# Performance work log

Hardware: AMD Instinct MI355X
Metric: run time of the kernel (lower is better)

## Reference

```python
import jax, jax.numpy as jnp
import numpy as np
from jax import lax


def _conv2d(x, w, pad=1):
    # x: (N,C,H,W), w: (O,I,kh,kw) -> (N,O,H,W)
    return lax.conv_general_dilated(
        x, w, window_strides=(1, 1), padding=[(pad, pad), (pad, pad)],
        dimension_numbers=("NCHW", "OIHW", "NCHW"))


def setup_inputs() -> dict:
    key = jax.random.key(0)
    ks = jax.random.split(key, 5)
    B, T, C, H, W = 4, 8, 256, 64, 64
    DH = 128
    fan = C * 3 * 3
    x = jax.random.normal(ks[0], (B, T, C, H, W), dtype=jnp.float32)
    w_k = jax.random.normal(ks[1], (DH, C, 3, 3), dtype=jnp.float32) * (2.0 / fan) ** 0.5
    w_q = jax.random.normal(ks[2], (DH, C, 3, 3), dtype=jnp.float32) * (2.0 / fan) ** 0.5
    w_v = jax.random.normal(ks[3], (DH, C, 3, 3), dtype=jnp.float32) * (2.0 / fan) ** 0.5
    w_out = jax.random.normal(ks[4], (C, DH, 3, 3), dtype=jnp.float32) * (2.0 / (DH * 9)) ** 0.5
    b_out = jnp.zeros((C,), dtype=jnp.float32)
    return {"x": x, "w_k": w_k, "w_q": w_q, "w_v": w_v, "w_out": w_out, "b_out": b_out}


def reference(x, w_k, w_q, w_v, w_out, b_out):
    B, T, C, H, W = x.shape
    DH = w_k.shape[0]
    # key comes only from the first frame
    k = _conv2d(x[:, 0], w_k)                                  # (B,DH,H,W)
    xf = x.reshape(B * T, C, H, W)
    q = _conv2d(xf, w_q).reshape(B, T, DH, H, W)               # (B,T,DH,H,W)
    v = _conv2d(xf, w_v).reshape(B, T, DH, H, W)
    # per-pixel channel dot between each frame's q and the single k
    dots = jnp.einsum("btchw,bchw->bthw", q, k)                # (B,T,H,W)
    attn = jax.nn.softmax(dots, axis=1)                        # softmax over T
    pooled = jnp.einsum("bthw,btchw->bchw", attn, v)           # (B,DH,H,W)
    # out conv applied once (result is identical for every repeated frame)
    out = _conv2d(pooled, w_out) + b_out[None, :, None, None]  # (B,C,H,W)
    return jnp.broadcast_to(out[:, None], (B, T, C, H, W))
```

## Files before the change

kernel.cpp:

```cpp
#include <hip/hip_runtime.h>
#include <cstdint>
#include <cstddef>

#define NB 4
#define NT 8
#define NC 256
#define NDH 128
#define HWs 4096

typedef _Float16 f16;
typedef _Float16 f16x8 __attribute__((ext_vector_type(8)));
typedef float f32x16 __attribute__((ext_vector_type(16)));


__device__ __forceinline__ void gload16(const void* g, void* l) {
    __builtin_amdgcn_global_load_lds(
        (const __attribute__((address_space(1))) void*)g,
        (__attribute__((address_space(3))) void*)l, 16, 0, 0);
}

__device__ __forceinline__ int xcd_swz(int bid, int nwg) {
    int q = nwg >> 3;
    return (bid & 7) * q + (bid >> 3);
}

__global__ __launch_bounds__(256) void prep_x_kernel(const float* __restrict__ x,
                                                     f16* __restrict__ xh) {
    __shared__ f16 sxt[256 * 66];
    int bt = blockIdx.x >> 6, h = blockIdx.x & 63;
    int tid = threadIdx.x;
    int w = tid & 63, c4 = tid >> 6;
    for (int p = 0; p < 64; ++p) {
        int c = p * 4 + c4;
        sxt[c * 66 + w] = (f16)x[(((size_t)bt * NC + c) * 64 + h) * 64 + w];
    }
    __syncthreads();
    int cg = tid & 31, wb = tid >> 5;
    f16x8* xh8 = (f16x8*)xh;
    for (int p = 0; p < 8; ++p) {
        int w2 = wb * 8 + p;
        f16x8 v;
        #pragma unroll
        for (int j = 0; j < 8; ++j) v[j] = sxt[(cg * 8 + j) * 66 + w2];
        xh8[((size_t)(bt * 64 + h) * 64 + w2) * 32 + cg] = v;
    }
}

__global__ __launch_bounds__(256) void prep_w_kernel(const float* __restrict__ w,
                                                     f16* __restrict__ wt2,
                                                     int OC, int CIN) {
    int CG = CIN >> 3;
    int idx = blockIdx.x * 256 + threadIdx.x;
    if (idx >= OC * CG) return;
    int oc = idx / CG, cg = idx - oc * CG;
    f16x8* wt8 = (f16x8*)wt2;
    #pragma unroll
    for (int tap = 0; tap < 9; ++tap) {
        f16x8 v;
        #pragma unroll
        for (int j = 0; j < 8; ++j)
            v[j] = (f16)w[((size_t)oc * CIN + cg * 8 + j) * 9 + tap];
        wt8[((size_t)tap * CG + cg) * OC + oc] = v;
    }
}

template <int CIN>
__device__ __forceinline__ void conv_core4(const f16x8* __restrict__ xh8,
                                           const f16x8* __restrict__ wt8,
                                           int OCT, int oc0, int h0,
                                           f16x8* __restrict__ sxb,
                                           f16x8* __restrict__ swb,
                                           f32x16 acc[2][2][2]) {
    const int tid = threadIdx.x;
    const int lane = tid & 63;
    const int wv = tid >> 6;
    const int ocg = wv >> 2, rp = wv & 3;
    const int n = lane & 31, q = lane >> 5;
    const int CG = CIN / 8;
    const int NI = CIN / 16;

    #pragma unroll
    for (int oi = 0; oi < 2; ++oi)
        #pragma unroll
        for (int rr = 0; rr < 2; ++rr)
            #pragma unroll
            for (int ct = 0; ct < 2; ++ct)
                #pragma unroll
                for (int r = 0; r < 16; ++r) acc[oi][rr][ct][r] = 0.0f;

    f16x8 Z8 = {(f16)0, (f16)0, (f16)0, (f16)0, (f16)0, (f16)0, (f16)0, (f16)0};

    if (tid < 80) {
        int buf = tid / 40, rem = tid - buf * 40;
        int r = rem >> 2, k = rem & 3;
        sxb[buf * 1320 + r * 132 + (k >> 1) * 130 + (k & 1)] = Z8;
    }
    if (h0 == 0 && tid < 264) {
        int buf = tid / 132, c = tid - buf * 132;
        sxb[buf * 1320 + c] = Z8;
    }
    if (h0 == 56 && tid < 264) {
        int buf = tid / 132, c = tid - buf * 132;
        sxb[buf * 1320 + 9 * 132 + c] = Z8;
    }

    auto stage = [&](f16x8* sx8, f16x8* sw8, int cg0) {
        for (int j = wv; j < 36; j += 8) {
            int tap = j >> 2, qh = (j >> 1) & 1, hf = j & 1;
            gload16(wt8 + (size_t)(tap * CG + cg0 + qh) * OCT + oc0 + hf * 64 + lane,
                    sw8 + (tap * 2 + qh) * 128 + hf * 64);
        }
        for (int j = wv; j < 20; j += 8) {
            int r = j >> 1, cb = j & 1;
            int h = h0 - 1 + r;
            if ((unsigned)h < 64u) {
                int col = cb * 32 + (lane >> 1);
                int cidx = col + 1;
                int cg = cg0 + ((lane & 1) ^ ((cidx >> 2) & 1));
                gload16(xh8 + (size_t)(h * 64 + col) * CG + cg,
                        sx8 + r * 132 + 2 + cb * 64);
            }
        }
    };

    stage(sxb, swb, 0);
    __syncthreads();

    for (int it = 0; it < NI; ++it) {
        f16x8* sx8 = sxb + (it & 1) * 1320;
        f16x8* sw8 = swb + (it & 1) * 2304;
        if (it + 1 < NI)
            stage(sxb + ((it + 1) & 1) * 1320, swb + ((it + 1) & 1) * 2304,
                  (it + 1) * 2);

        __builtin_amdgcn_s_setprio(1);
        #pragma unroll
        for (int kx = 0; kx < 3; ++kx) {
            f16x8 bb[4][2];
            #pragma unroll
            for (int j = 0; j < 4; ++j) {
                const int r = rp * 2 + j;
                #pragma unroll
                for (int ct = 0; ct < 2; ++ct) {
                    int cidx = ct * 32 + n + kx;
                    int s = q ^ ((cidx >> 2) & 1);
                    bb[j][ct] = sx8[r * 132 + cidx * 2 + s];
                }
            }
            #pragma unroll
            for (int ky = 0; ky < 3; ++ky) {
                const int tap = ky * 3 + kx;
                f16x8 a0 = sw8[(tap * 2 + q) * 128 + ocg * 64 + n];
                f16x8 a1 = sw8[(tap * 2 + q) * 128 + ocg * 64 + 32 + n];
                #pragma unroll
                for (int rr = 0; rr < 2; ++rr) {
                    #pragma unroll
                    for (int ct = 0; ct < 2; ++ct) {
                        f16x8 b = bb[rr + ky][ct];
                        acc[0][rr][ct] = __builtin_amdgcn_mfma_f32_32x32x16_f16(a0, b, acc[0][rr][ct], 0, 0, 0);
                        acc[1][rr][ct] = __builtin_amdgcn_mfma_f32_32x32x16_f16(a1, b, acc[1][rr][ct], 0, 0, 0);
                    }
                }
            }
        }
        __builtin_amdgcn_s_setprio(0);
        __syncthreads();
    }
}

__global__ __launch_bounds__(512, 2) void conv_k_kernel(const f16* __restrict__ xh,
        const f16* __restrict__ wk2, float* __restrict__ kbuf) {
    __shared__ f16x8 sxb[2 * 1320];
    __shared__ f16x8 swb[2 * 2304];
    int s = xcd_swz(blockIdx.x, NB * 8);
    int b = s >> 3, hb = s & 7;
    int h0 = hb * 8;
    int bt = b * NT;
    f32x16 acc[2][2][2];
    conv_core4<NC>((const f16x8*)xh + (size_t)bt * 64 * 64 * 32, (const f16x8*)wk2,
                   NDH, 0, h0, sxb, swb, acc);
    int lane = threadIdx.x & 63, wv = threadIdx.x >> 6;
    int ocg = wv >> 2, rp = wv & 3;
    int n = lane & 31, q = lane >> 5;
    #pragma unroll
    for (int rr = 0; rr < 2; ++rr) {
        int h = h0 + rp * 2 + rr;
        #pragma unroll
        for (int oi = 0; oi < 2; ++oi)
            #pragma unroll
            for (int r = 0; r < 16; ++r) {
                int oc = ocg * 64 + oi * 32 + 4 * q + (r & 3) + 8 * (r >> 2);
                float* kp = kbuf + ((size_t)(b * NDH + oc)) * HWs + h * 64;
                kp[n] = acc[oi][rr][0][r];
                kp[32 + n] = acc[oi][rr][1][r];
            }
    }
}

__global__ __launch_bounds__(512, 2) void conv_q_kernel(const f16* __restrict__ xh,
        const f16* __restrict__ wq2, const float* __restrict__ kbuf,
        float* __restrict__ qpart) {
    __shared__ f16x8 sxb[2 * 1320];
    __shared__ f16x8 swb[2 * 2304];
    int s = xcd_swz(blockIdx.x, NB * NT * 8);
    int bt = s >> 3, hb = s & 7;
    int b = bt >> 3;
    int h0 = hb * 8;
    f32x16 acc[2][2][2];
    conv_core4<NC>((const f16x8*)xh + (size_t)bt * 64 * 64 * 32, (const f16x8*)wq2,
                   NDH, 0, h0, sxb, swb, acc);
    int lane = threadIdx.x & 63, wv = threadIdx.x >> 6;
    int ocg = wv >> 2, rp = wv & 3;
    int n = lane & 31, q = lane >> 5;
    #pragma unroll
    for (int rr = 0; rr < 2; ++rr) {
        int h = h0 + rp * 2 + rr;
        float p0 = 0.0f, p1 = 0.0f;
        #pragma unroll
        for (int oi = 0; oi < 2; ++oi)
            #pragma unroll
            for (int r = 0; r < 16; ++r) {
                int oc = ocg * 64 + oi * 32 + 4 * q + (r & 3) + 8 * (r >> 2);
                const float* kp = kbuf + ((size_t)(b * NDH + oc)) * HWs + h * 64;
                p0 += acc[oi][rr][0][r] * kp[n];
                p1 += acc[oi][rr][1][r] * kp[32 + n];
            }
        p0 += __shfl_xor(p0, 32, 64);
        p1 += __shfl_xor(p1, 32, 64);
        if (q == 0) {
            qpart[((size_t)ocg * 32 + bt) * HWs + h * 64 + n] = p0;
            qpart[((size_t)ocg * 32 + bt) * HWs + h * 64 + 32 + n] = p1;
        }
    }
}

__global__ __launch_bounds__(256) void softmax_t_kernel(const float* __restrict__ qpart,
                                                        float* __restrict__ dots) {
    int idx = blockIdx.x * 256 + threadIdx.x;
    int b = idx >> 12;
    int p = idx & 4095;
    const float* q0 = qpart + (size_t)(b * NT) * HWs + p;
    const float* q1 = qpart + (size_t)(32 + b * NT) * HWs + p;
    float v[NT];
    float m = -3.4e38f;
    #pragma unroll
    for (int t = 0; t < NT; ++t) { v[t] = q0[t * HWs] + q1[t * HWs]; m = fmaxf(m, v[t]); }
    float s = 0.0f;
    #pragma unroll
    for (int t = 0; t < NT; ++t) { v[t] = __expf(v[t] - m); s += v[t]; }
    float inv = 1.0f / s;
    float* base = dots + (size_t)b * NT * HWs + p;
    #pragma unroll
    for (int t = 0; t < NT; ++t) base[t * HWs] = v[t] * inv;
}

__global__ __launch_bounds__(512, 2) void conv_v_kernel(const f16* __restrict__ xh,
        const f16* __restrict__ wv2, const float* __restrict__ attn,
        f16* __restrict__ parts) {
    __shared__ f16x8 sxb[2 * 1320];
    __shared__ f16x8 swb[2 * 2304];
    int s = xcd_swz(blockIdx.x, NB * NT * 8);
    int bt = s >> 3, hb = s & 7;
    int b = bt >> 3, t = bt & 7;
    int h0 = hb * 8;
    f32x16 acc[2][2][2];
    conv_core4<NC>((const f16x8*)xh + (size_t)bt * 64 * 64 * 32, (const f16x8*)wv2,
                   NDH, 0, h0, sxb, swb, acc);
    int lane = threadIdx.x & 63, wv = threadIdx.x >> 6;
    int ocg = wv >> 2, rp = wv & 3;
    int n = lane & 31, q = lane >> 5;
    f16* pp = parts + (size_t)(t * NB + b) * NDH * HWs;
    #pragma unroll
    for (int rr = 0; rr < 2; ++rr) {
        int h = h0 + rp * 2 + rr;
        float a0 = attn[(size_t)bt * HWs + h * 64 + n];
        float a1 = attn[(size_t)bt * HWs + h * 64 + 32 + n];
        #pragma unroll
        for (int oi = 0; oi < 2; ++oi)
            #pragma unroll
            for (int r = 0; r < 16; ++r) {
                int oc = ocg * 64 + oi * 32 + 4 * q + (r & 3) + 8 * (r >> 2);
                f16* op = pp + (size_t)oc * HWs + h * 64;
                op[n] = (f16)(a0 * acc[oi][rr][0][r]);
                op[32 + n] = (f16)(a1 * acc[oi][rr][1][r]);
            }
    }
}

__global__ __launch_bounds__(256) void prep_pooled_kernel(const f16* __restrict__ parts,
                                                          f16* __restrict__ pooledT) {
    __shared__ f16 sxt[128 * 66];
    int b = blockIdx.x >> 6, h = blockIdx.x & 63;
    int tid = threadIdx.x, w = tid & 63, c4 = tid >> 6;
    for (int p = 0; p < 32; ++p) {
        int c = p * 4 + c4;
        float s = 0.0f;
        #pragma unroll
        for (int t = 0; t < NT; ++t)
            s += (float)parts[(((size_t)(t * NB + b) * NDH + c)) * HWs + h * 64 + w];
        sxt[c * 66 + w] = (f16)s;
    }
    __syncthreads();
    int cg = tid & 15, wb = tid >> 4;
    f16x8* pt8 = (f16x8*)pooledT;
    for (int p = 0; p < 4; ++p) {
        int w2 = wb * 4 + p;
        f16x8 v;
        #pragma unroll
        for (int j = 0; j < 8; ++j) v[j] = sxt[(cg * 8 + j) * 66 + w2];
        pt8[((size_t)(b * 64 + h) * 64 + w2) * 16 + cg] = v;
    }
}

__global__ __launch_bounds__(512, 2) void conv_out_kernel(const f16* __restrict__ pooledT,
        const f16* __restrict__ wo2, const float* __restrict__ b_out,
        float* __restrict__ out) {
    __shared__ f16x8 sxb[2 * 1320];
    __shared__ f16x8 swb[2 * 2304];
    int s = xcd_swz(blockIdx.x, NB * 2 * 8);
    int b = s >> 4, oh = (s >> 3) & 1, hb = s & 7;
    int h0 = hb * 8, oc0 = oh * 128;
    f32x16 acc[2][2][2];
    conv_core4<NDH>((const f16x8*)pooledT + (size_t)b * 64 * 64 * 16, (const f16x8*)wo2,
                    NC, oc0, h0, sxb, swb, acc);
    int lane = threadIdx.x & 63, wv = threadIdx.x >> 6;
    int ocg = wv >> 2, rp = wv & 3;
    int n = lane & 31, q = lane >> 5;
    #pragma unroll
    for (int rr = 0; rr < 2; ++rr) {
        int h = h0 + rp * 2 + rr;
        #pragma unroll
        for (int oi = 0; oi < 2; ++oi)
            #pragma unroll
            for (int r = 0; r < 16; ++r) {
                int oc = oc0 + ocg * 64 + oi * 32 + 4 * q + (r & 3) + 8 * (r >> 2);
                float bias = b_out[oc];
                float v0 = acc[oi][rr][0][r] + bias;
                float v1 = acc[oi][rr][1][r] + bias;
                for (int t = 0; t < NT; ++t) {
                    float* op = out + ((size_t)(b * NT + t) * NC + oc) * HWs + h * 64;
                    op[n] = v0;
                    op[32 + n] = v1;
                }
            }
    }
}

extern "C" void kernel_launch(void* const* d_in, const int* in_sizes, int n_in,
                              void* d_out, int out_size, void* d_ws, size_t ws_size,
                              hipStream_t stream) {
    (void)in_sizes; (void)n_in; (void)out_size; (void)ws_size;
    const float* x     = (const float*)d_in[0];
    const float* w_k   = (const float*)d_in[1];
    const float* w_q   = (const float*)d_in[2];
    const float* w_v   = (const float*)d_in[3];
    const float* w_out = (const float*)d_in[4];
    const float* b_out = (const float*)d_in[5];
    float* out = (float*)d_out;

    char* ws = (char*)d_ws;
    f16*   xh      = (f16*)ws;
    float* kbuf    = (float*)(ws + 67108864);
    float* dots    = (float*)(ws + 75497472);
    f16*   parts   = (f16*)(ws + 76021760);
    float* qpart   = (float*)(ws + 76021760);
    f16*   pooledT = (f16*)(ws + 109576192);
    f16*   wq2     = (f16*)(ws + 113770496);
    f16*   wk2     = (f16*)(ws + 114360320);
    f16*   wv2     = (f16*)(ws + 114950144);
    f16*   wo2     = (f16*)(ws + 115539968);

    hipLaunchKernelGGL(prep_x_kernel, dim3(2048), dim3(256), 0, stream, x, xh);
    hipLaunchKernelGGL(prep_w_kernel, dim3(16), dim3(256), 0, stream, w_q, wq2, NDH, NC);
    hipLaunchKernelGGL(prep_w_kernel, dim3(16), dim3(256), 0, stream, w_k, wk2, NDH, NC);
    hipLaunchKernelGGL(prep_w_kernel, dim3(16), dim3(256), 0, stream, w_v, wv2, NDH, NC);
    hipLaunchKernelGGL(prep_w_kernel, dim3(16), dim3(256), 0, stream, w_out, wo2, NC, NDH);

    hipLaunchKernelGGL(conv_k_kernel, dim3(NB * 8), dim3(512), 0, stream, xh, wk2, kbuf);
    hipLaunchKernelGGL(conv_q_kernel, dim3(NB * NT * 8), dim3(512), 0, stream, xh, wq2, kbuf, qpart);
    hipLaunchKernelGGL(softmax_t_kernel, dim3(64), dim3(256), 0, stream, qpart, dots);
    hipLaunchKernelGGL(conv_v_kernel, dim3(NB * NT * 8), dim3(512), 0, stream, xh, wv2, dots, parts);
    hipLaunchKernelGGL(prep_pooled_kernel, dim3(256), dim3(256), 0, stream, parts, pooledT);
    hipLaunchKernelGGL(conv_out_kernel, dim3(NB * 2 * 8), dim3(512), 0, stream, pooledT, wo2, b_out, out);
}
```

Before: 540.6 us.

## Split-K the key conv across blocks and double-buffer B fragments in conv core

The key conv previously ran on only 32 blocks. It is now split four ways over input channels into 128 blocks that write partial sums, followed by a new reduce kernel that sums the partials into kbuf. The shared conv core also restructures its LDS reads: B fragments for the next kx shift are prefetched into alternating register sets, and A fragments for all ky are loaded up front. The aim is better occupancy on the small k conv and better overlap of LDS reads with MFMA. The cost is an extra 32 MB partial buffer round-trip, an extra launch, and higher register pressure.

```diff
diff --git a/kernel.cpp b/kernel.cpp
--- a/kernel.cpp
+++ b/kernel.cpp
@@ -65,9 +65,10 @@
 }
 
 template <int CIN>
-__device__ __forceinline__ void conv_core4(const f16x8* __restrict__ xh8,
+__device__ __forceinline__ void conv_core5(const f16x8* __restrict__ xh8,
                                            const f16x8* __restrict__ wt8,
                                            int OCT, int oc0, int h0,
+                                           int cg_base, int ni,
                                            f16x8* __restrict__ sxb,
                                            f16x8* __restrict__ swb,
                                            f32x16 acc[2][2][2]) {
@@ -77,7 +78,6 @@
     const int ocg = wv >> 2, rp = wv & 3;
     const int n = lane & 31, q = lane >> 5;
     const int CG = CIN / 8;
-    const int NI = CIN / 16;
 
     #pragma unroll
     for (int oi = 0; oi < 2; ++oi)
@@ -123,42 +123,55 @@
         }
     };
 
-    stage(sxb, swb, 0);
+    stage(sxb, swb, cg_base);
     __syncthreads();
 
-    for (int it = 0; it < NI; ++it) {
+    for (int it = 0; it < ni; ++it) {
         f16x8* sx8 = sxb + (it & 1) * 1320;
         f16x8* sw8 = swb + (it & 1) * 2304;
-        if (it + 1 < NI)
+        if (it + 1 < ni)
             stage(sxb + ((it + 1) & 1) * 1320, swb + ((it + 1) & 1) * 2304,
-                  (it + 1) * 2);
+                  cg_base + (it + 1) * 2);
 
         __builtin_amdgcn_s_setprio(1);
+        f16x8 bbA[4][2], bbB[4][2];
+        #pragma unroll
+        for (int j = 0; j < 4; ++j)
+            #pragma unroll
+            for (int ct = 0; ct < 2; ++ct) {
+                int cidx = ct * 32 + n;
+                int s = q ^ ((cidx >> 2) & 1);
+                bbA[j][ct] = sx8[(rp * 2 + j) * 132 + cidx * 2 + s];
+            }
         #pragma unroll
         for (int kx = 0; kx < 3; ++kx) {
-            f16x8 bb[4][2];
-            #pragma unroll
-            for (int j = 0; j < 4; ++j) {
-                const int r = rp * 2 + j;
-                #pragma unroll
-                for (int ct = 0; ct < 2; ++ct) {
-                    int cidx = ct * 32 + n + kx;
-                    int s = q ^ ((cidx >> 2) & 1);
-                    bb[j][ct] = sx8[r * 132 + cidx * 2 + s];
-                }
-            }
+            f16x8 aa[3][2];
             #pragma unroll
             for (int ky = 0; ky < 3; ++ky) {
                 const int tap = ky * 3 + kx;
-                f16x8 a0 = sw8[(tap * 2 + q) * 128 + ocg * 64 + n];
-                f16x8 a1 = sw8[(tap * 2 + q) * 128 + ocg * 64 + 32 + n];
+                aa[ky][0] = sw8[(tap * 2 + q) * 128 + ocg * 64 + n];
+                aa[ky][1] = sw8[(tap * 2 + q) * 128 + ocg * 64 + 32 + n];
+            }
+            if (kx < 2) {
+                #pragma unroll
+                for (int j = 0; j < 4; ++j)
+                    #pragma unroll
+                    for (int ct = 0; ct < 2; ++ct) {
+                        int cidx = ct * 32 + n + kx + 1;
+                        int s = q ^ ((cidx >> 2) & 1);
+                        f16x8 v = sx8[(rp * 2 + j) * 132 + cidx * 2 + s];
+                        if (kx & 1) bbA[j][ct] = v; else bbB[j][ct] = v;
+                    }
+            }
+            #pragma unroll
+            for (int ky = 0; ky < 3; ++ky) {
                 #pragma unroll
                 for (int rr = 0; rr < 2; ++rr) {
                     #pragma unroll
                     for (int ct = 0; ct < 2; ++ct) {
-                        f16x8 b = bb[rr + ky][ct];
-                        acc[0][rr][ct] = __builtin_amdgcn_mfma_f32_32x32x16_f16(a0, b, acc[0][rr][ct], 0, 0, 0);
-                        acc[1][rr][ct] = __builtin_amdgcn_mfma_f32_32x32x16_f16(a1, b, acc[1][rr][ct], 0, 0, 0);
+                        f16x8 b = (kx & 1) ? bbB[rr + ky][ct] : bbA[rr + ky][ct];
+                        acc[0][rr][ct] = __builtin_amdgcn_mfma_f32_32x32x16_f16(aa[ky][0], b, acc[0][rr][ct], 0, 0, 0);
+                        acc[1][rr][ct] = __builtin_amdgcn_mfma_f32_32x32x16_f16(aa[ky][1], b, acc[1][rr][ct], 0, 0, 0);
                     }
                 }
             }
@@ -169,16 +182,16 @@
 }
 
 __global__ __launch_bounds__(512, 2) void conv_k_kernel(const f16* __restrict__ xh,
-        const f16* __restrict__ wk2, float* __restrict__ kbuf) {
+        const f16* __restrict__ wk2, float* __restrict__ kpart) {
     __shared__ f16x8 sxb[2 * 1320];
     __shared__ f16x8 swb[2 * 2304];
-    int s = xcd_swz(blockIdx.x, NB * 8);
-    int b = s >> 3, hb = s & 7;
+    int s = xcd_swz(blockIdx.x, NB * 8 * 4);
+    int b = s >> 5, hb = (s >> 2) & 7, ks = s & 3;
     int h0 = hb * 8;
     int bt = b * NT;
     f32x16 acc[2][2][2];
-    conv_core4<NC>((const f16x8*)xh + (size_t)bt * 64 * 64 * 32, (const f16x8*)wk2,
-                   NDH, 0, h0, sxb, swb, acc);
+    conv_core5<NC>((const f16x8*)xh + (size_t)bt * 64 * 64 * 32, (const f16x8*)wk2,
+                   NDH, 0, h0, ks * 8, 4, sxb, swb, acc);
     int lane = threadIdx.x & 63, wv = threadIdx.x >> 6;
     int ocg = wv >> 2, rp = wv & 3;
     int n = lane & 31, q = lane >> 5;
@@ -190,11 +203,27 @@
             #pragma unroll
             for (int r = 0; r < 16; ++r) {
                 int oc = ocg * 64 + oi * 32 + 4 * q + (r & 3) + 8 * (r >> 2);
-                float* kp = kbuf + ((size_t)(b * NDH + oc)) * HWs + h * 64;
+                float* kp = kpart + ((size_t)((ks * NB + b) * NDH + oc)) * HWs + h * 64;
                 kp[n] = acc[oi][rr][0][r];
                 kp[32 + n] = acc[oi][rr][1][r];
             }
     }
+}
+
+__global__ __launch_bounds__(256) void reduce_k_kernel(const float* __restrict__ kpart,
+                                                       float* __restrict__ kbuf) {
+    int idx = blockIdx.x * 256 + threadIdx.x;
+    const float4* p = (const float4*)kpart;
+    float4 v0 = p[idx];
+    float4 v1 = p[idx + 524288];
+    float4 v2 = p[idx + 2 * 524288];
+    float4 v3 = p[idx + 3 * 524288];
+    float4 o;
+    o.x = v0.x + v1.x + v2.x + v3.x;
+    o.y = v0.y + v1.y + v2.y + v3.y;
+    o.z = v0.z + v1.z + v2.z + v3.z;
+    o.w = v0.w + v1.w + v2.w + v3.w;
+    ((float4*)kbuf)[idx] = o;
 }
 
 __global__ __launch_bounds__(512, 2) void conv_q_kernel(const f16* __restrict__ xh,
@@ -207,8 +236,8 @@
     int b = bt >> 3;
     int h0 = hb * 8;
     f32x16 acc[2][2][2];
-    conv_core4<NC>((const f16x8*)xh + (size_t)bt * 64 * 64 * 32, (const f16x8*)wq2,
-                   NDH, 0, h0, sxb, swb, acc);
+    conv_core5<NC>((const f16x8*)xh + (size_t)bt * 64 * 64 * 32, (const f16x8*)wq2,
+                   NDH, 0, h0, 0, 16, sxb, swb, acc);
     int lane = threadIdx.x & 63, wv = threadIdx.x >> 6;
     int ocg = wv >> 2, rp = wv & 3;
     int n = lane & 31, q = lane >> 5;
@@ -264,8 +293,8 @@
     int b = bt >> 3, t = bt & 7;
     int h0 = hb * 8;
     f32x16 acc[2][2][2];
-    conv_core4<NC>((const f16x8*)xh + (size_t)bt * 64 * 64 * 32, (const f16x8*)wv2,
-                   NDH, 0, h0, sxb, swb, acc);
+    conv_core5<NC>((const f16x8*)xh + (size_t)bt * 64 * 64 * 32, (const f16x8*)wv2,
+                   NDH, 0, h0, 0, 16, sxb, swb, acc);
     int lane = threadIdx.x & 63, wv = threadIdx.x >> 6;
     int ocg = wv >> 2, rp = wv & 3;
     int n = lane & 31, q = lane >> 5;
@@ -321,8 +350,8 @@
     int b = s >> 4, oh = (s >> 3) & 1, hb = s & 7;
     int h0 = hb * 8, oc0 = oh * 128;
     f32x16 acc[2][2][2];
-    conv_core4<NDH>((const f16x8*)pooledT + (size_t)b * 64 * 64 * 16, (const f16x8*)wo2,
-                    NC, oc0, h0, sxb, swb, acc);
+    conv_core5<NDH>((const f16x8*)pooledT + (size_t)b * 64 * 64 * 16, (const f16x8*)wo2,
+                    NC, oc0, h0, 0, 8, sxb, swb, acc);
     int lane = threadIdx.x & 63, wv = threadIdx.x >> 6;
     int ocg = wv >> 2, rp = wv & 3;
     int n = lane & 31, q = lane >> 5;
@@ -363,6 +392,7 @@
     float* kbuf    = (float*)(ws + 67108864);
     float* dots    = (float*)(ws + 75497472);
     f16*   parts   = (f16*)(ws + 76021760);
+    float* kpart   = (float*)(ws + 76021760);
     float* qpart   = (float*)(ws + 76021760);
     f16*   pooledT = (f16*)(ws + 109576192);
     f16*   wq2     = (f16*)(ws + 113770496);
@@ -376,7 +406,8 @@
     hipLaunchKernelGGL(prep_w_kernel, dim3(16), dim3(256), 0, stream, w_v, wv2, NDH, NC);
     hipLaunchKernelGGL(prep_w_kernel, dim3(16), dim3(256), 0, stream, w_out, wo2, NC, NDH);
 
-    hipLaunchKernelGGL(conv_k_kernel, dim3(NB * 8), dim3(512), 0, stream, xh, wk2, kbuf);
+    hipLaunchKernelGGL(conv_k_kernel, dim3(NB * 8 * 4), dim3(512), 0, stream, xh, wk2, kpart);
+    hipLaunchKernelGGL(reduce_k_kernel, dim3(2048), dim3(256), 0, stream, kpart, kbuf);
     hipLaunchKernelGGL(conv_q_kernel, dim3(NB * NT * 8), dim3(512), 0, stream, xh, wq2, kbuf, qpart);
     hipLaunchKernelGGL(softmax_t_kernel, dim3(64), dim3(256), 0, stream, qpart, dots);
     hipLaunchKernelGGL(conv_v_kernel, dim3(NB * NT * 8), dim3(512), 0, stream, xh, wv2, dots, parts);
```

New measurement: 507.6 us. 6.1% less time.
